# Kernel optimization log

Hardware: AMD Instinct MI355X
Metric: run time of the kernel (lower is better)

## Reference

```python
import jax, jax.numpy as jnp
import numpy as np

B, T, OBS = 256, 200, 128
H, L, S = 128, 32, 50


def setup_inputs() -> dict:
    key = jax.random.key(0)
    ks = jax.random.split(key, 10)
    sc_in = 1.0 / np.sqrt(OBS + L)
    sc_h = 1.0 / np.sqrt(H)
    return {
        "inputs": jax.random.normal(ks[0], (B, T, OBS), dtype=jnp.float32),
        "eps": jax.random.normal(ks[1], (T, B * S, L), dtype=jnp.float32),
        "W_ih": jax.random.normal(ks[2], (4 * H, OBS + L), dtype=jnp.float32) * sc_in,
        "W_hh": jax.random.normal(ks[3], (4 * H, H), dtype=jnp.float32) * sc_h,
        "b_ih": jax.random.normal(ks[4], (4 * H,), dtype=jnp.float32) * 0.01,
        "b_hh": jax.random.normal(ks[5], (4 * H,), dtype=jnp.float32) * 0.01,
        "W_mu": jax.random.normal(ks[6], (L, H), dtype=jnp.float32) * sc_h,
        "b_mu": jax.random.normal(ks[7], (L,), dtype=jnp.float32) * 0.01,
        "cov_diag": jax.random.uniform(ks[8], (L,), dtype=jnp.float32, minval=0.5, maxval=1.5),
        "num_samples": S,
    }


def reference(inputs, eps, W_ih, W_hh, b_ih, b_hh, W_mu, b_mu, cov_diag, num_samples):
    batch, num_steps, _ = inputs.shape
    hid = b_ih.shape[0] // 4
    lat = b_mu.shape[0]
    BS = batch * num_samples

    std = jnp.sqrt(cov_diag)                       # [L], state-independent diag cov
    logdet = jnp.sum(jnp.log(cov_diag))
    TWO_PI = 2.0 * jnp.pi
    ent_const = 0.5 * lat * (1.0 + jnp.log(TWO_PI)) + 0.5 * logdet

    # tile([num_samples, 1]) in torch repeats the whole batch block -> sample-major
    x_tiled = jnp.tile(inputs.transpose(1, 0, 2), (1, num_samples, 1))  # [T, BS, obs]

    def step(carry, xs):
        h, c, z_prev = carry
        x_t, eps_t = xs
        rnn_in = jnp.concatenate([x_t, z_prev], axis=-1)          # [BS, obs+L]
        gates = rnn_in @ W_ih.T + b_ih + h @ W_hh.T + b_hh        # [BS, 4H]
        i, f, g, o = jnp.split(gates, 4, axis=-1)
        c_new = jax.nn.sigmoid(f) * c + jax.nn.sigmoid(i) * jnp.tanh(g)
        h_new = jax.nn.sigmoid(o) * jnp.tanh(c_new)
        mean = h_new @ W_mu.T + b_mu                              # [BS, L]
        z = mean + eps_t * std                                    # reparam sample
        ent = jnp.broadcast_to(ent_const, (z.shape[0],))          # diag-MVN entropy
        # log N(z; mean, diag(cov)) with (z-mean)/std == eps_t
        lp = -0.5 * (jnp.sum(eps_t * eps_t, axis=-1) + lat * jnp.log(TWO_PI) + logdet)
        return (h_new, c_new, z), (z, ent, lp)

    init = (
        jnp.zeros((BS, hid), dtype=inputs.dtype),
        jnp.zeros((BS, hid), dtype=inputs.dtype),
        jnp.zeros((BS, lat), dtype=inputs.dtype),
    )
    _, (zs, ents, lps) = jax.lax.scan(step, init, (x_tiled, eps))  # [T,BS,L],[T,BS],[T,BS]

    sampled_s = zs.transpose(1, 0, 2).reshape(num_samples, batch, num_steps, lat)
    entropies = ents.T.reshape(num_samples, batch, num_steps)
    log_probs = lps.T.reshape(num_samples, batch, num_steps)
    return sampled_s, entropies, log_probs
```

## Files before the change

### kernel.cpp

```cpp
#include <hip/hip_runtime.h>
#include <stdint.h>

#define T_STEPS 200
#define OBSD    128
#define HID     128
#define LATD    32
#define BS_TOT  12800
#define KIN     160

#define OUT_ENT_OFF 81920000
#define OUT_LP_OFF  84480000

#define WR_OFF  0
#define H_OFF   131072
#define WMU_OFF 147456
#define E_OFF   155648
#define LDS_SZ  159744

#define L2E  1.4426950408889634f
#define L2E2 2.8853900817779268f
#define LOG2PI 1.8378770664093453f

typedef short  bf16x8 __attribute__((ext_vector_type(8)));
typedef float  f32x4  __attribute__((ext_vector_type(4)));
typedef uint32_t u32;

__device__ __forceinline__ uint16_t f2bf(float f) {
    u32 u = __builtin_bit_cast(u32, f);
    u32 r = (u + 0x7fffu + ((u >> 16) & 1u)) >> 16;
    return (uint16_t)r;
}
__device__ __forceinline__ float bf2f(u32 bits16) {
    u32 u = bits16 << 16;
    return __builtin_bit_cast(float, u);
}
__device__ __forceinline__ u32 pack2(float a, float b) {
    return (u32)f2bf(a) | ((u32)f2bf(b) << 16);
}
__device__ __forceinline__ u32 cvt_pk_bf16(float lo, float hi) {
    u32 r;
    asm("v_cvt_pk_bf16_f32 %0, %1, %2" : "=v"(r) : "v"(lo), "v"(hi));
    return r;
}
__device__ __forceinline__ float sig2(float x) {
    float e;
    asm("v_exp_f32 %0, -%1" : "=v"(e) : "v"(x));
    return __builtin_amdgcn_rcpf(1.f + e);
}
__device__ __forceinline__ float tanh2(float x) {
    float e;
    asm("v_exp_f32 %0, %1" : "=v"(e) : "v"(x));
    return 1.f - 2.f * __builtin_amdgcn_rcpf(1.f + e);
}
__device__ __forceinline__ int hswz(int row, int col) {
    return ((row << 8) + (col << 1)) ^ ((row & 7) << 4);
}

__global__ __launch_bounds__(512, 2) void xg_prep(
    const float* __restrict__ x,
    const float* __restrict__ W_ih,
    const float* __restrict__ b_ih,
    const float* __restrict__ b_hh,
    const float* __restrict__ b_mu,
    uint16_t* __restrict__ xg)
{
    const int blk = blockIdx.x;
    const int t   = blk >> 2, bq = blk & 3;
    const int tid = threadIdx.x;
    const int w = tid >> 6, l = tid & 63, lg = l >> 4, ln = l & 15;
    const int b0 = bq * 64;

    bf16x8 wb[4][4];
    float  bias[4];
    #pragma unroll
    for (int q = 0; q < 4; ++q) {
        const int col = q * 128 + w * 16 + ln;
        float zb = 0.f;
        #pragma unroll
        for (int j = 0; j < 32; ++j) zb += b_mu[j] * W_ih[col * KIN + 128 + j];
        bias[q] = b_ih[col] + b_hh[col] + (t > 0 ? zb : 0.f);
        #pragma unroll
        for (int ks = 0; ks < 4; ++ks) {
            bf16x8 v;
            #pragma unroll
            for (int e = 0; e < 8; ++e)
                v[e] = (short)f2bf(W_ih[col * KIN + ks * 32 + lg * 8 + e]);
            wb[ks][q] = v;
        }
    }

    f32x4 acc[4][4];
    const f32x4 vz = {0.f, 0.f, 0.f, 0.f};
    #pragma unroll
    for (int rt = 0; rt < 4; ++rt)
        #pragma unroll
        for (int q = 0; q < 4; ++q) acc[rt][q] = vz;

    #pragma unroll
    for (int ks = 0; ks < 4; ++ks) {
        bf16x8 a[4];
        #pragma unroll
        for (int rt = 0; rt < 4; ++rt) {
            const int brow = b0 + rt * 16 + ln;
            const float* src = x + ((size_t)brow * T_STEPS + t) * OBSD + ks * 32 + lg * 8;
            bf16x8 v;
            #pragma unroll
            for (int e = 0; e < 8; ++e) v[e] = (short)f2bf(src[e]);
            a[rt] = v;
        }
        #pragma unroll
        for (int rt = 0; rt < 4; ++rt)
            #pragma unroll
            for (int q = 0; q < 4; ++q)
                acc[rt][q] = __builtin_amdgcn_mfma_f32_16x16x32_bf16(
                    a[rt], wb[ks][q], acc[rt][q], 0, 0, 0);
    }

    const float gsc[4] = {L2E, L2E, L2E2, L2E};
    uint4* dst = (uint4*)xg + ((size_t)blk * 512 + tid) * 8;
    #pragma unroll
    for (int rt = 0; rt < 4; ++rt) {
        float v0[4], v1[4], v2[4], v3[4];
        #pragma unroll
        for (int e = 0; e < 4; ++e) {
            v0[e] = (acc[rt][0][e] + bias[0]) * gsc[0];
            v1[e] = (acc[rt][1][e] + bias[1]) * gsc[1];
            v2[e] = (acc[rt][2][e] + bias[2]) * gsc[2];
            v3[e] = (acc[rt][3][e] + bias[3]) * gsc[3];
        }
        uint4 o0, o1;
        o0.x = pack2(v0[0], v0[1]); o0.y = pack2(v0[2], v0[3]);
        o0.z = pack2(v1[0], v1[1]); o0.w = pack2(v1[2], v1[3]);
        o1.x = pack2(v2[0], v2[1]); o1.y = pack2(v2[2], v2[3]);
        o1.z = pack2(v3[0], v3[1]); o1.w = pack2(v3[2], v3[3]);
        dst[2 * rt]     = o0;
        dst[2 * rt + 1] = o1;
    }
}

__global__ __launch_bounds__(256) void lp_ent(
    const float* __restrict__ eps,
    const float* __restrict__ cov,
    float* __restrict__ out)
{
    const int blk = blockIdx.x;
    const int rc = blk >> 2, tq = blk & 3;
    const int tid = threadIdx.x;
    const int c = tid & 3, rl = tid >> 2;
    const int row = rc * 64 + rl;

    float logdet = 0.f;
    for (int i = 0; i < LATD; ++i) logdet += logf(cov[i]);
    const float lconst = 32.f * LOG2PI + logdet;
    const float ec = 0.5f * 32.f * (1.f + LOG2PI) + 0.5f * logdet;

    const int t0 = tq * 50;
    for (int t = t0; t < t0 + 50; ++t) {
        const float* ep = eps + ((size_t)t * BS_TOT + row) * LATD + c * 8;
        const float4 a0 = *(const float4*)ep;
        const float4 a1 = *(const float4*)(ep + 4);
        float ps = a0.x*a0.x + a0.y*a0.y + a0.z*a0.z + a0.w*a0.w
                 + a1.x*a1.x + a1.y*a1.y + a1.z*a1.z + a1.w*a1.w;
        ps += __shfl_xor(ps, 1, 64);
        ps += __shfl_xor(ps, 2, 64);
        if (c == 0) {
            out[OUT_LP_OFF  + (size_t)row * 200 + t] = -0.5f * (ps + lconst);
            out[OUT_ENT_OFF + (size_t)row * 200 + t] = ec;
        }
    }
}

__global__ __launch_bounds__(1024, 4) void lstm_main(
    const float* __restrict__ eps,
    const float* __restrict__ W_ih,
    const float* __restrict__ W_hh,
    const float* __restrict__ W_mu,
    const float* __restrict__ b_mu,
    const float* __restrict__ cov,
    const uint16_t* __restrict__ xg,
    float* __restrict__ out)
{
    __shared__ __align__(16) char smem[LDS_SZ];

    const int tid = threadIdx.x;
    const int w = tid >> 6, l = tid & 63, lg = l >> 4, ln = l & 15;
    const int wp = w & 7, half = w >> 3;

    const int xcd = blockIdx.x & 7;
    const int wk  = (xcd >> 1) + 4 * ((blockIdx.x >> 3) + 25 * (xcd & 1));
    const int bq  = wk & 3;
    const int bs0 = wk * 64;

    {
        float* ws = (float*)(smem + H_OFF);
        for (int i = tid; i < 4096; i += 1024) ws[i] = W_mu[i];
    }
    __syncthreads();
    const float* wmu_s = (const float*)(smem + H_OFF);

    for (int i = tid; i < 2048; i += 1024) {
        const int col = i >> 6, k2 = (i & 63) * 2;
        const u32 p = pack2(wmu_s[col * HID + k2], wmu_s[col * HID + k2 + 1]);
        *(u32*)(smem + WMU_OFF + (((col << 8) + (k2 << 1)) ^ ((col & 7) << 4))) = p;
    }

    bf16x8 weg[4];
    {
        float stds[8];
        #pragma unroll
        for (int e = 0; e < 8; ++e) stds[e] = sqrtf(cov[lg * 8 + e]);
        const float gsc[4] = {L2E, L2E, L2E2, L2E};
        #pragma unroll
        for (int q = 0; q < 4; ++q) {
            const int col = q * 128 + wp * 16 + ln;
            bf16x8 v;
            #pragma unroll
            for (int e = 0; e < 8; ++e)
                v[e] = (short)f2bf(W_ih[col * KIN + 128 + lg * 8 + e] * stds[e] * gsc[q]);
            weg[q] = v;
        }
    }

    #pragma unroll
    for (int qq = 0; qq < 2; ++qq) {
        const int q = half * 2 + qq;
        const float gs = (q == 2) ? L2E2 : L2E;
        const int col = q * 128 + wp * 16 + ln;
        float wzf[32];
        #pragma unroll
        for (int j4 = 0; j4 < 8; ++j4)
            *(float4*)&wzf[j4 * 4] = *(const float4*)&W_ih[col * KIN + 128 + j4 * 4];
        #pragma unroll
        for (int ks = 0; ks < 4; ++ks) {
            float base[8];
            *(float4*)&base[0] = *(const float4*)&W_hh[col * HID + ks * 32 + lg * 8];
            *(float4*)&base[4] = *(const float4*)&W_hh[col * HID + ks * 32 + lg * 8 + 4];
            bf16x8 v;
            #pragma unroll
            for (int e = 0; e < 8; ++e) {
                float s = base[e];
                #pragma unroll
                for (int j = 0; j < 32; ++j)
                    s += wzf[j] * wmu_s[j * HID + ks * 32 + lg * 8 + e];
                v[e] = (short)f2bf(s * gs);
            }
            *(bf16x8*)(smem + WR_OFF + (((ks * 4 + q) * 8 + wp) << 10) + l * 16) = v;
        }
    }

    const int rtm = (w >> 1) & 3, ctm = w & 1;
    const int zcol = ctm * 16 + ln;
    const float stdv = sqrtf(cov[zcol]);
    const float bmu  = b_mu[zcol];

    __syncthreads();

    for (int i = tid; i < 4096; i += 1024) ((u32*)(smem + H_OFF))[i] = 0;
    for (int i = tid; i < 1024; i += 1024) ((u32*)(smem + E_OFF))[i] = 0;

    const f32x4 vz4 = {0.f, 0.f, 0.f, 0.f};
    f32x4 cst[2] = {vz4, vz4};

    const int erow = tid >> 4, ecol = (tid & 15) * 2;
    const int ewr = ((erow >> 4) * 64 + (ecol >> 3) * 16 + (erow & 15)) * 16 + (ecol & 7) * 2;

    __syncthreads();

    for (int t = 0; t < T_STEPS; ++t) {
        uint4 xv[4];
        const uint4* xp = (const uint4*)xg
            + ((size_t)(t * 4 + bq) * 512 + wp * 64 + l) * 8 + half * 4;
        #pragma unroll
        for (int i = 0; i < 4; ++i) xv[i] = xp[i];
        const float2 fev = *(const float2*)(eps + ((size_t)t * BS_TOT + bs0 + erow) * LATD + ecol);

        f32x4 acc[2][4];
        #pragma unroll
        for (int rt = 0; rt < 2; ++rt) {
            const bf16x8 aE = *(const bf16x8*)(smem + E_OFF + (((half * 2 + rt) * 64 + l) << 4));
            #pragma unroll
            for (int q = 0; q < 4; ++q)
                acc[rt][q] = __builtin_amdgcn_mfma_f32_16x16x32_bf16(
                    aE, weg[q], vz4, 0, 0, 0);
        }
        #pragma unroll
        for (int ks = 0; ks < 4; ++ks) {
            bf16x8 bfr[4];
            #pragma unroll
            for (int q = 0; q < 4; ++q)
                bfr[q] = *(const bf16x8*)(smem + WR_OFF + (((ks * 4 + q) * 8 + wp) << 10) + l * 16);
            bf16x8 a[2];
            #pragma unroll
            for (int rt = 0; rt < 2; ++rt)
                a[rt] = *(const bf16x8*)(smem + H_OFF + hswz((half * 2 + rt) * 16 + ln, ks * 32 + lg * 8));
            #pragma unroll
            for (int rt = 0; rt < 2; ++rt)
                #pragma unroll
                for (int q = 0; q < 4; ++q)
                    acc[rt][q] = __builtin_amdgcn_mfma_f32_16x16x32_bf16(
                        a[rt], bfr[q], acc[rt][q], 0, 0, 0);
        }
        if (half == 0 && t > 0) {
            f32x4 macc = vz4;
            #pragma unroll
            for (int ks = 0; ks < 4; ++ks) {
                const bf16x8 am = *(const bf16x8*)(smem + H_OFF + hswz(rtm * 16 + ln, ks * 32 + lg * 8));
                const bf16x8 bm = *(const bf16x8*)(smem + WMU_OFF + hswz(zcol, ks * 32 + lg * 8));
                macc = __builtin_amdgcn_mfma_f32_16x16x32_bf16(am, bm, macc, 0, 0, 0);
            }
            #pragma unroll
            for (int e = 0; e < 4; ++e) {
                const int row = rtm * 16 + lg * 4 + e;
                const int eb = (rtm * 64 + (zcol >> 3) * 16 + (lg * 4 + e)) * 16 + (zcol & 7) * 2;
                const float evv = bf2f(*(const uint16_t*)(smem + E_OFF + eb));
                out[(size_t)(bs0 + row) * 6400 + (t - 1) * 32 + zcol] =
                    macc[e] + bmu + evv * stdv;
            }
        }

        __syncthreads();

        *(u32*)(smem + E_OFF + ewr) = cvt_pk_bf16(fev.x, fev.y);

        #pragma unroll
        for (int rt = 0; rt < 2; ++rt) {
            const uint4 u01 = xv[2 * rt], u23 = xv[2 * rt + 1];
            const float xi[4] = { bf2f(u01.x & 0xffff), bf2f(u01.x >> 16),
                                  bf2f(u01.y & 0xffff), bf2f(u01.y >> 16) };
            const float xf[4] = { bf2f(u01.z & 0xffff), bf2f(u01.z >> 16),
                                  bf2f(u01.w & 0xffff), bf2f(u01.w >> 16) };
            const float xgv[4] = { bf2f(u23.x & 0xffff), bf2f(u23.x >> 16),
                                   bf2f(u23.y & 0xffff), bf2f(u23.y >> 16) };
            const float xo[4] = { bf2f(u23.z & 0xffff), bf2f(u23.z >> 16),
                                  bf2f(u23.w & 0xffff), bf2f(u23.w >> 16) };
            #pragma unroll
            for (int e = 0; e < 4; ++e) {
                const float iv = acc[rt][0][e] + xi[e];
                const float fv = acc[rt][1][e] + xf[e];
                const float gv = acc[rt][2][e] + xgv[e];
                const float ov = acc[rt][3][e] + xo[e];
                const float c  = sig2(fv) * cst[rt][e] + sig2(iv) * tanh2(gv);
                cst[rt][e] = c;
                const float h = sig2(ov) * tanh2(c * L2E2);
                const int row = (half * 2 + rt) * 16 + lg * 4 + e;
                *(uint16_t*)(smem + H_OFF + hswz(row, wp * 16 + ln)) = f2bf(h);
            }
        }

        __syncthreads();
    }

    if (half == 0) {
        f32x4 macc = vz4;
        #pragma unroll
        for (int ks = 0; ks < 4; ++ks) {
            const bf16x8 am = *(const bf16x8*)(smem + H_OFF + hswz(rtm * 16 + ln, ks * 32 + lg * 8));
            const bf16x8 bm = *(const bf16x8*)(smem + WMU_OFF + hswz(zcol, ks * 32 + lg * 8));
            macc = __builtin_amdgcn_mfma_f32_16x16x32_bf16(am, bm, macc, 0, 0, 0);
        }
        #pragma unroll
        for (int e = 0; e < 4; ++e) {
            const int row = rtm * 16 + lg * 4 + e;
            const int eb = (rtm * 64 + (zcol >> 3) * 16 + (lg * 4 + e)) * 16 + (zcol & 7) * 2;
            const float evv = bf2f(*(const uint16_t*)(smem + E_OFF + eb));
            out[(size_t)(bs0 + row) * 6400 + 199 * 32 + zcol] =
                macc[e] + bmu + evv * stdv;
        }
    }
}

extern "C" void kernel_launch(void* const* d_in, const int* in_sizes, int n_in,
                              void* d_out, int out_size, void* d_ws, size_t ws_size,
                              hipStream_t stream) {
    const float* x    = (const float*)d_in[0];
    const float* eps  = (const float*)d_in[1];
    const float* W_ih = (const float*)d_in[2];
    const float* W_hh = (const float*)d_in[3];
    const float* b_ih = (const float*)d_in[4];
    const float* b_hh = (const float*)d_in[5];
    const float* W_mu = (const float*)d_in[6];
    const float* b_mu = (const float*)d_in[7];
    const float* cov  = (const float*)d_in[8];
    float* out = (float*)d_out;
    uint16_t* xg = (uint16_t*)d_ws;

    hipLaunchKernelGGL(xg_prep, dim3(800), dim3(512), 0, stream, x, W_ih, b_ih, b_hh, b_mu, xg);
    hipLaunchKernelGGL(lp_ent, dim3(800), dim3(256), 0, stream, eps, cov, out);
    hipLaunchKernelGGL(lstm_main, dim3(200), dim3(1024), 0, stream,
                       eps, W_ih, W_hh, W_mu, b_mu, cov, xg, out);
}
```

Measured before the change: 1.811 ms.

## Hold recurrent weights in registers with 512-thread blocks and double-buffered LDS

The LSTM recurrence kernel drops from 16 to 8 waves per block. Each wave now covers all 64 rows and keeps its fused W_hh+W_ih·W_mu slice in registers (wr[4][4]) instead of reading it from LDS every step. The hidden-state and eps tiles are double-buffered in LDS, so the two per-step __syncthreads become a single lgkmcnt wait plus barrier. This removes weight LDS traffic and one barrier per timestep. In exchange it raises register pressure, since accumulators, cell state and x loads all double, and halves thread-level parallelism.

```diff
diff --git a/kernel.cpp b/kernel.cpp
--- a/kernel.cpp
+++ b/kernel.cpp
@@ -11,11 +11,10 @@
 #define OUT_ENT_OFF 81920000
 #define OUT_LP_OFF  84480000
 
-#define WR_OFF  0
-#define H_OFF   131072
-#define WMU_OFF 147456
-#define E_OFF   155648
-#define LDS_SZ  159744
+#define H0_OFF  0
+#define WMU_OFF 32768
+#define E0_OFF  40960
+#define LDS_SZ  49152
 
 #define L2E  1.4426950408889634f
 #define L2E2 2.8853900817779268f
@@ -24,6 +23,13 @@
 typedef short  bf16x8 __attribute__((ext_vector_type(8)));
 typedef float  f32x4  __attribute__((ext_vector_type(4)));
 typedef uint32_t u32;
+
+#define BAR() do {                                        \
+    __builtin_amdgcn_sched_barrier(0);                    \
+    asm volatile("s_waitcnt lgkmcnt(0)" ::: "memory");    \
+    __builtin_amdgcn_s_barrier();                         \
+    __builtin_amdgcn_sched_barrier(0);                    \
+} while (0)
 
 __device__ __forceinline__ uint16_t f2bf(float f) {
     u32 u = __builtin_bit_cast(u32, f);
@@ -170,7 +176,7 @@
     }
 }
 
-__global__ __launch_bounds__(1024, 4) void lstm_main(
+__global__ __launch_bounds__(512, 2) void lstm_main(
     const float* __restrict__ eps,
     const float* __restrict__ W_ih,
     const float* __restrict__ W_hh,
@@ -184,7 +190,6 @@
 
     const int tid = threadIdx.x;
     const int w = tid >> 6, l = tid & 63, lg = l >> 4, ln = l & 15;
-    const int wp = w & 7, half = w >> 3;
 
     const int xcd = blockIdx.x & 7;
     const int wk  = (xcd >> 1) + 4 * ((blockIdx.x >> 3) + 25 * (xcd & 1));
@@ -192,13 +197,13 @@
     const int bs0 = wk * 64;
 
     {
-        float* ws = (float*)(smem + H_OFF);
-        for (int i = tid; i < 4096; i += 1024) ws[i] = W_mu[i];
+        float* ws = (float*)(smem + H0_OFF);
+        for (int i = tid; i < 4096; i += 512) ws[i] = W_mu[i];
     }
     __syncthreads();
-    const float* wmu_s = (const float*)(smem + H_OFF);
-
-    for (int i = tid; i < 2048; i += 1024) {
+    const float* wmu_s = (const float*)(smem + H0_OFF);
+
+    for (int i = tid; i < 2048; i += 512) {
         const int col = i >> 6, k2 = (i & 63) * 2;
         const u32 p = pack2(wmu_s[col * HID + k2], wmu_s[col * HID + k2 + 1]);
         *(u32*)(smem + WMU_OFF + (((col << 8) + (k2 << 1)) ^ ((col & 7) << 4))) = p;
@@ -212,7 +217,7 @@
         const float gsc[4] = {L2E, L2E, L2E2, L2E};
         #pragma unroll
         for (int q = 0; q < 4; ++q) {
-            const int col = q * 128 + wp * 16 + ln;
+            const int col = q * 128 + w * 16 + ln;
             bf16x8 v;
             #pragma unroll
             for (int e = 0; e < 8; ++e)
@@ -221,11 +226,11 @@
         }
     }
 
+    bf16x8 wr[4][4];
     #pragma unroll
-    for (int qq = 0; qq < 2; ++qq) {
-        const int q = half * 2 + qq;
+    for (int q = 0; q < 4; ++q) {
         const float gs = (q == 2) ? L2E2 : L2E;
-        const int col = q * 128 + wp * 16 + ln;
+        const int col = q * 128 + w * 16 + ln;
         float wzf[32];
         #pragma unroll
         for (int j4 = 0; j4 < 8; ++j4)
@@ -244,40 +249,46 @@
                     s += wzf[j] * wmu_s[j * HID + ks * 32 + lg * 8 + e];
                 v[e] = (short)f2bf(s * gs);
             }
-            *(bf16x8*)(smem + WR_OFF + (((ks * 4 + q) * 8 + wp) << 10) + l * 16) = v;
-        }
-    }
-
-    const int rtm = (w >> 1) & 3, ctm = w & 1;
+            wr[ks][q] = v;
+        }
+    }
+
+    const int rtm = w >> 1, ctm = w & 1;
     const int zcol = ctm * 16 + ln;
     const float stdv = sqrtf(cov[zcol]);
     const float bmu  = b_mu[zcol];
 
     __syncthreads();
 
-    for (int i = tid; i < 4096; i += 1024) ((u32*)(smem + H_OFF))[i] = 0;
-    for (int i = tid; i < 1024; i += 1024) ((u32*)(smem + E_OFF))[i] = 0;
+    for (int i = tid; i < 4096; i += 512) ((u32*)(smem + H0_OFF))[i] = 0;
+    for (int i = tid; i < 1024; i += 512) ((u32*)(smem + E0_OFF))[i] = 0;
 
     const f32x4 vz4 = {0.f, 0.f, 0.f, 0.f};
-    f32x4 cst[2] = {vz4, vz4};
-
-    const int erow = tid >> 4, ecol = (tid & 15) * 2;
-    const int ewr = ((erow >> 4) * 64 + (ecol >> 3) * 16 + (erow & 15)) * 16 + (ecol & 7) * 2;
+    f32x4 cst[4] = {vz4, vz4, vz4, vz4};
+
+    const int erow = tid >> 3, ecol = (tid & 7) * 4;
+    const int ert = erow >> 4;
+    const int ewr = ((ert * 64 + (ecol >> 3) * 16 + (erow & 15)) << 4) + (ecol & 7) * 2;
 
     __syncthreads();
 
     for (int t = 0; t < T_STEPS; ++t) {
-        uint4 xv[4];
-        const uint4* xp = (const uint4*)xg
-            + ((size_t)(t * 4 + bq) * 512 + wp * 64 + l) * 8 + half * 4;
-        #pragma unroll
-        for (int i = 0; i < 4; ++i) xv[i] = xp[i];
-        const float2 fev = *(const float2*)(eps + ((size_t)t * BS_TOT + bs0 + erow) * LATD + ecol);
-
-        f32x4 acc[2][4];
-        #pragma unroll
-        for (int rt = 0; rt < 2; ++rt) {
-            const bf16x8 aE = *(const bf16x8*)(smem + E_OFF + (((half * 2 + rt) * 64 + l) << 4));
+        const int pb = t & 1;
+        const char* Hp = smem + H0_OFF + pb * 16384;
+        char*       Hn = smem + H0_OFF + (pb ^ 1) * 16384;
+        const char* Ep = smem + E0_OFF + pb * 4096;
+        char*       En = smem + E0_OFF + (pb ^ 1) * 4096;
+
+        uint4 xv[8];
+        const uint4* xp = (const uint4*)xg + ((size_t)(t * 4 + bq) * 512 + tid) * 8;
+        #pragma unroll
+        for (int i = 0; i < 8; ++i) xv[i] = xp[i];
+        const float4 fe = *(const float4*)(eps + ((size_t)t * BS_TOT + bs0 + erow) * LATD + ecol);
+
+        f32x4 acc[4][4];
+        #pragma unroll
+        for (int rt = 0; rt < 4; ++rt) {
+            const bf16x8 aE = *(const bf16x8*)(Ep + ((rt * 64 + l) << 4));
             #pragma unroll
             for (int q = 0; q < 4; ++q)
                 acc[rt][q] = __builtin_amdgcn_mfma_f32_16x16x32_bf16(
@@ -285,45 +296,37 @@
         }
         #pragma unroll
         for (int ks = 0; ks < 4; ++ks) {
-            bf16x8 bfr[4];
-            #pragma unroll
-            for (int q = 0; q < 4; ++q)
-                bfr[q] = *(const bf16x8*)(smem + WR_OFF + (((ks * 4 + q) * 8 + wp) << 10) + l * 16);
-            bf16x8 a[2];
-            #pragma unroll
-            for (int rt = 0; rt < 2; ++rt)
-                a[rt] = *(const bf16x8*)(smem + H_OFF + hswz((half * 2 + rt) * 16 + ln, ks * 32 + lg * 8));
-            #pragma unroll
-            for (int rt = 0; rt < 2; ++rt)
+            bf16x8 a[4];
+            #pragma unroll
+            for (int rt = 0; rt < 4; ++rt)
+                a[rt] = *(const bf16x8*)(Hp + hswz(rt * 16 + ln, ks * 32 + lg * 8));
+            #pragma unroll
+            for (int rt = 0; rt < 4; ++rt)
                 #pragma unroll
                 for (int q = 0; q < 4; ++q)
                     acc[rt][q] = __builtin_amdgcn_mfma_f32_16x16x32_bf16(
-                        a[rt], bfr[q], acc[rt][q], 0, 0, 0);
-        }
-        if (half == 0 && t > 0) {
+                        a[rt], wr[ks][q], acc[rt][q], 0, 0, 0);
+        }
+        if (t > 0) {
             f32x4 macc = vz4;
             #pragma unroll
             for (int ks = 0; ks < 4; ++ks) {
-                const bf16x8 am = *(const bf16x8*)(smem + H_OFF + hswz(rtm * 16 + ln, ks * 32 + lg * 8));
+                const bf16x8 am = *(const bf16x8*)(Hp + hswz(rtm * 16 + ln, ks * 32 + lg * 8));
                 const bf16x8 bm = *(const bf16x8*)(smem + WMU_OFF + hswz(zcol, ks * 32 + lg * 8));
                 macc = __builtin_amdgcn_mfma_f32_16x16x32_bf16(am, bm, macc, 0, 0, 0);
             }
             #pragma unroll
             for (int e = 0; e < 4; ++e) {
                 const int row = rtm * 16 + lg * 4 + e;
-                const int eb = (rtm * 64 + (zcol >> 3) * 16 + (lg * 4 + e)) * 16 + (zcol & 7) * 2;
-                const float evv = bf2f(*(const uint16_t*)(smem + E_OFF + eb));
+                const float evv = bf2f(*(const uint16_t*)(
+                    Ep + ((rtm * 64 + (zcol >> 3) * 16 + (lg * 4 + e)) << 4) + (zcol & 7) * 2));
                 out[(size_t)(bs0 + row) * 6400 + (t - 1) * 32 + zcol] =
                     macc[e] + bmu + evv * stdv;
             }
         }
 
-        __syncthreads();
-
-        *(u32*)(smem + E_OFF + ewr) = cvt_pk_bf16(fev.x, fev.y);
-
-        #pragma unroll
-        for (int rt = 0; rt < 2; ++rt) {
+        #pragma unroll
+        for (int rt = 0; rt < 4; ++rt) {
             const uint4 u01 = xv[2 * rt], u23 = xv[2 * rt + 1];
             const float xi[4] = { bf2f(u01.x & 0xffff), bf2f(u01.x >> 16),
                                   bf2f(u01.y & 0xffff), bf2f(u01.y >> 16) };
@@ -342,27 +345,36 @@
                 const float c  = sig2(fv) * cst[rt][e] + sig2(iv) * tanh2(gv);
                 cst[rt][e] = c;
                 const float h = sig2(ov) * tanh2(c * L2E2);
-                const int row = (half * 2 + rt) * 16 + lg * 4 + e;
-                *(uint16_t*)(smem + H_OFF + hswz(row, wp * 16 + ln)) = f2bf(h);
+                const int row = rt * 16 + lg * 4 + e;
+                *(uint16_t*)(Hn + hswz(row, w * 16 + ln)) = f2bf(h);
             }
         }
 
-        __syncthreads();
-    }
-
-    if (half == 0) {
+        {
+            uint2 p;
+            p.x = cvt_pk_bf16(fe.x, fe.y);
+            p.y = cvt_pk_bf16(fe.z, fe.w);
+            *(uint2*)(En + ewr) = p;
+        }
+
+        BAR();
+    }
+
+    {
+        const char* Hp = smem + H0_OFF + (T_STEPS & 1) * 16384;
+        const char* Ep = smem + E0_OFF + (T_STEPS & 1) * 4096;
         f32x4 macc = vz4;
         #pragma unroll
         for (int ks = 0; ks < 4; ++ks) {
-            const bf16x8 am = *(const bf16x8*)(smem + H_OFF + hswz(rtm * 16 + ln, ks * 32 + lg * 8));
+            const bf16x8 am = *(const bf16x8*)(Hp + hswz(rtm * 16 + ln, ks * 32 + lg * 8));
             const bf16x8 bm = *(const bf16x8*)(smem + WMU_OFF + hswz(zcol, ks * 32 + lg * 8));
             macc = __builtin_amdgcn_mfma_f32_16x16x32_bf16(am, bm, macc, 0, 0, 0);
         }
         #pragma unroll
         for (int e = 0; e < 4; ++e) {
             const int row = rtm * 16 + lg * 4 + e;
-            const int eb = (rtm * 64 + (zcol >> 3) * 16 + (lg * 4 + e)) * 16 + (zcol & 7) * 2;
-            const float evv = bf2f(*(const uint16_t*)(smem + E_OFF + eb));
+            const float evv = bf2f(*(const uint16_t*)(
+                Ep + ((rtm * 64 + (zcol >> 3) * 16 + (lg * 4 + e)) << 4) + (zcol & 7) * 2));
             out[(size_t)(bs0 + row) * 6400 + 199 * 32 + zcol] =
                 macc[e] + bmu + evv * stdv;
         }
@@ -386,6 +398,6 @@
 
     hipLaunchKernelGGL(xg_prep, dim3(800), dim3(512), 0, stream, x, W_ih, b_ih, b_hh, b_mu, xg);
     hipLaunchKernelGGL(lp_ent, dim3(800), dim3(256), 0, stream, eps, cov, out);
-    hipLaunchKernelGGL(lstm_main, dim3(200), dim3(1024), 0, stream,
+    hipLaunchKernelGGL(lstm_main, dim3(200), dim3(512), 0, stream,
                        eps, W_ih, W_hh, W_mu, b_mu, cov, xg, out);
 }
```

New measurement: 1.824 ms. No clear change (+0.7%).

## Fuse lp/entropy into LSTM grid, double-buffer h, hold weights in registers

Applied to the files above, without the earlier changes.

Removes the separate lp_ent kernel and runs its work on 56 extra blocks of the main LSTM launch, using CUs left idle by the 200 recurrent blocks. The recurrent loop double-buffers the h state in LDS so each step needs one barrier instead of two. Eps is now fed to the MFMA from registers instead of staged through LDS, and the xg precomputed gates are folded in as the MFMA accumulator init. Half of the recurrent weight tiles move from LDS into registers to cut LDS traffic. This raises register pressure and removes the dependency ordering between the two former kernels.

```diff
diff --git a/kernel.cpp b/kernel.cpp
--- a/kernel.cpp
+++ b/kernel.cpp
@@ -12,10 +12,9 @@
 #define OUT_LP_OFF  84480000
 
 #define WR_OFF  0
-#define H_OFF   131072
-#define WMU_OFF 147456
-#define E_OFF   155648
-#define LDS_SZ  159744
+#define H_OFF   65536
+#define WMU_OFF 98304
+#define LDS_SZ  106496
 
 #define L2E  1.4426950408889634f
 #define L2E2 2.8853900817779268f
@@ -24,6 +23,14 @@
 typedef short  bf16x8 __attribute__((ext_vector_type(8)));
 typedef float  f32x4  __attribute__((ext_vector_type(4)));
 typedef uint32_t u32;
+typedef u32    u32x4  __attribute__((ext_vector_type(4)));
+
+#define BAR() do {                                        \
+    __builtin_amdgcn_sched_barrier(0);                    \
+    asm volatile("s_waitcnt lgkmcnt(0)" ::: "memory");    \
+    __builtin_amdgcn_s_barrier();                         \
+    __builtin_amdgcn_sched_barrier(0);                    \
+} while (0)
 
 __device__ __forceinline__ uint16_t f2bf(float f) {
     u32 u = __builtin_bit_cast(u32, f);
@@ -54,6 +61,14 @@
 }
 __device__ __forceinline__ int hswz(int row, int col) {
     return ((row << 8) + (col << 1)) ^ ((row & 7) << 4);
+}
+__device__ __forceinline__ f32x4 cfrag(u32 u01, u32 u23) {
+    f32x4 c;
+    c[0] = __builtin_bit_cast(float, u01 << 16);
+    c[1] = __builtin_bit_cast(float, u01 & 0xffff0000u);
+    c[2] = __builtin_bit_cast(float, u23 << 16);
+    c[3] = __builtin_bit_cast(float, u23 & 0xffff0000u);
+    return c;
 }
 
 __global__ __launch_bounds__(512, 2) void xg_prep(
@@ -138,38 +153,6 @@
     }
 }
 
-__global__ __launch_bounds__(256) void lp_ent(
-    const float* __restrict__ eps,
-    const float* __restrict__ cov,
-    float* __restrict__ out)
-{
-    const int blk = blockIdx.x;
-    const int rc = blk >> 2, tq = blk & 3;
-    const int tid = threadIdx.x;
-    const int c = tid & 3, rl = tid >> 2;
-    const int row = rc * 64 + rl;
-
-    float logdet = 0.f;
-    for (int i = 0; i < LATD; ++i) logdet += logf(cov[i]);
-    const float lconst = 32.f * LOG2PI + logdet;
-    const float ec = 0.5f * 32.f * (1.f + LOG2PI) + 0.5f * logdet;
-
-    const int t0 = tq * 50;
-    for (int t = t0; t < t0 + 50; ++t) {
-        const float* ep = eps + ((size_t)t * BS_TOT + row) * LATD + c * 8;
-        const float4 a0 = *(const float4*)ep;
-        const float4 a1 = *(const float4*)(ep + 4);
-        float ps = a0.x*a0.x + a0.y*a0.y + a0.z*a0.z + a0.w*a0.w
-                 + a1.x*a1.x + a1.y*a1.y + a1.z*a1.z + a1.w*a1.w;
-        ps += __shfl_xor(ps, 1, 64);
-        ps += __shfl_xor(ps, 2, 64);
-        if (c == 0) {
-            out[OUT_LP_OFF  + (size_t)row * 200 + t] = -0.5f * (ps + lconst);
-            out[OUT_ENT_OFF + (size_t)row * 200 + t] = ec;
-        }
-    }
-}
-
 __global__ __launch_bounds__(1024, 4) void lstm_main(
     const float* __restrict__ eps,
     const float* __restrict__ W_ih,
@@ -183,6 +166,28 @@
     __shared__ __align__(16) char smem[LDS_SZ];
 
     const int tid = threadIdx.x;
+
+    if (blockIdx.x >= 200) {
+        float logdet = 0.f;
+        for (int i = 0; i < LATD; ++i) logdet += logf(cov[i]);
+        const float lconst = 32.f * LOG2PI + logdet;
+        const float ec = 0.5f * 32.f * (1.f + LOG2PI) + 0.5f * logdet;
+        const int base = (blockIdx.x - 200) * 1024 + tid;
+        for (int j = base; j < T_STEPS * BS_TOT; j += 56 * 1024) {
+            const float* ep = eps + (size_t)j * LATD;
+            float ps = 0.f;
+            #pragma unroll
+            for (int k = 0; k < 8; ++k) {
+                const float4 a = *(const float4*)(ep + k * 4);
+                ps += a.x * a.x + a.y * a.y + a.z * a.z + a.w * a.w;
+            }
+            const int t = j / BS_TOT, row = j - t * BS_TOT;
+            out[OUT_LP_OFF  + (size_t)row * 200 + t] = -0.5f * (ps + lconst);
+            out[OUT_ENT_OFF + (size_t)row * 200 + t] = ec;
+        }
+        return;
+    }
+
     const int w = tid >> 6, l = tid & 63, lg = l >> 4, ln = l & 15;
     const int wp = w & 7, half = w >> 3;
 
@@ -221,9 +226,9 @@
         }
     }
 
+    bf16x8 wrr[2][4];
     #pragma unroll
-    for (int qq = 0; qq < 2; ++qq) {
-        const int q = half * 2 + qq;
+    for (int q = 0; q < 4; ++q) {
         const float gs = (q == 2) ? L2E2 : L2E;
         const int col = q * 128 + wp * 16 + ln;
         float wzf[32];
@@ -232,6 +237,7 @@
             *(float4*)&wzf[j4 * 4] = *(const float4*)&W_ih[col * KIN + 128 + j4 * 4];
         #pragma unroll
         for (int ks = 0; ks < 4; ++ks) {
+            if (ks < 2 && half != 0) continue;
             float base[8];
             *(float4*)&base[0] = *(const float4*)&W_hh[col * HID + ks * 32 + lg * 8];
             *(float4*)&base[4] = *(const float4*)&W_hh[col * HID + ks * 32 + lg * 8 + 4];
@@ -244,7 +250,10 @@
                     s += wzf[j] * wmu_s[j * HID + ks * 32 + lg * 8 + e];
                 v[e] = (short)f2bf(s * gs);
             }
-            *(bf16x8*)(smem + WR_OFF + (((ks * 4 + q) * 8 + wp) << 10) + l * 16) = v;
+            if (ks < 2)
+                *(bf16x8*)(smem + WR_OFF + (((ks * 4 + q) * 8 + wp) << 10) + l * 16) = v;
+            else
+                wrr[ks - 2][q] = v;
         }
     }
 
@@ -256,114 +265,128 @@
     __syncthreads();
 
     for (int i = tid; i < 4096; i += 1024) ((u32*)(smem + H_OFF))[i] = 0;
-    for (int i = tid; i < 1024; i += 1024) ((u32*)(smem + E_OFF))[i] = 0;
 
     const f32x4 vz4 = {0.f, 0.f, 0.f, 0.f};
     f32x4 cst[2] = {vz4, vz4};
-
-    const int erow = tid >> 4, ecol = (tid & 15) * 2;
-    const int ewr = ((erow >> 4) * 64 + (ecol >> 3) * 16 + (erow & 15)) * 16 + (ecol & 7) * 2;
+    u32x4 epf[2] = {{0, 0, 0, 0}, {0, 0, 0, 0}};
 
     __syncthreads();
 
     for (int t = 0; t < T_STEPS; ++t) {
+        const int pb = t & 1;
+        const char* Hp = smem + H_OFF + pb * 16384;
+        char*       Hn = smem + H_OFF + (pb ^ 1) * 16384;
+
         uint4 xv[4];
         const uint4* xp = (const uint4*)xg
             + ((size_t)(t * 4 + bq) * 512 + wp * 64 + l) * 8 + half * 4;
         #pragma unroll
         for (int i = 0; i < 4; ++i) xv[i] = xp[i];
-        const float2 fev = *(const float2*)(eps + ((size_t)t * BS_TOT + bs0 + erow) * LATD + ecol);
+        float4 fa[2], fb[2];
+        #pragma unroll
+        for (int rt = 0; rt < 2; ++rt) {
+            const float* ep = eps
+                + ((size_t)t * BS_TOT + bs0 + (half * 2 + rt) * 16 + ln) * LATD + lg * 8;
+            fa[rt] = *(const float4*)ep;
+            fb[rt] = *(const float4*)(ep + 4);
+        }
+        float ez[4];
+        if (half == 0) {
+            const size_t eb = (size_t)(t > 0 ? t - 1 : 0) * BS_TOT + bs0 + rtm * 16 + lg * 4;
+            #pragma unroll
+            for (int e = 0; e < 4; ++e) ez[e] = eps[(eb + e) * LATD + zcol];
+        }
 
         f32x4 acc[2][4];
         #pragma unroll
         for (int rt = 0; rt < 2; ++rt) {
-            const bf16x8 aE = *(const bf16x8*)(smem + E_OFF + (((half * 2 + rt) * 64 + l) << 4));
-            #pragma unroll
-            for (int q = 0; q < 4; ++q)
-                acc[rt][q] = __builtin_amdgcn_mfma_f32_16x16x32_bf16(
-                    aE, weg[q], vz4, 0, 0, 0);
+            const bf16x8 aE = __builtin_bit_cast(bf16x8, epf[rt]);
+            const uint4 ua = xv[2 * rt], ub = xv[2 * rt + 1];
+            acc[rt][0] = __builtin_amdgcn_mfma_f32_16x16x32_bf16(aE, weg[0], cfrag(ua.x, ua.y), 0, 0, 0);
+            acc[rt][1] = __builtin_amdgcn_mfma_f32_16x16x32_bf16(aE, weg[1], cfrag(ua.z, ua.w), 0, 0, 0);
+            acc[rt][2] = __builtin_amdgcn_mfma_f32_16x16x32_bf16(aE, weg[2], cfrag(ub.x, ub.y), 0, 0, 0);
+            acc[rt][3] = __builtin_amdgcn_mfma_f32_16x16x32_bf16(aE, weg[3], cfrag(ub.z, ub.w), 0, 0, 0);
         }
         #pragma unroll
         for (int ks = 0; ks < 4; ++ks) {
-            bf16x8 bfr[4];
-            #pragma unroll
-            for (int q = 0; q < 4; ++q)
-                bfr[q] = *(const bf16x8*)(smem + WR_OFF + (((ks * 4 + q) * 8 + wp) << 10) + l * 16);
             bf16x8 a[2];
             #pragma unroll
             for (int rt = 0; rt < 2; ++rt)
-                a[rt] = *(const bf16x8*)(smem + H_OFF + hswz((half * 2 + rt) * 16 + ln, ks * 32 + lg * 8));
-            #pragma unroll
-            for (int rt = 0; rt < 2; ++rt)
+                a[rt] = *(const bf16x8*)(Hp + hswz((half * 2 + rt) * 16 + ln, ks * 32 + lg * 8));
+            #pragma unroll
+            for (int q = 0; q < 4; ++q) {
+                bf16x8 bfr;
+                if (ks < 2)
+                    bfr = *(const bf16x8*)(smem + WR_OFF + (((ks * 4 + q) * 8 + wp) << 10) + l * 16);
+                else
+                    bfr = wrr[ks - 2][q];
                 #pragma unroll
-                for (int q = 0; q < 4; ++q)
+                for (int rt = 0; rt < 2; ++rt)
                     acc[rt][q] = __builtin_amdgcn_mfma_f32_16x16x32_bf16(
-                        a[rt], bfr[q], acc[rt][q], 0, 0, 0);
+                        a[rt], bfr, acc[rt][q], 0, 0, 0);
+            }
         }
         if (half == 0 && t > 0) {
             f32x4 macc = vz4;
             #pragma unroll
             for (int ks = 0; ks < 4; ++ks) {
-                const bf16x8 am = *(const bf16x8*)(smem + H_OFF + hswz(rtm * 16 + ln, ks * 32 + lg * 8));
+                const bf16x8 am = *(const bf16x8*)(Hp + hswz(rtm * 16 + ln, ks * 32 + lg * 8));
                 const bf16x8 bm = *(const bf16x8*)(smem + WMU_OFF + hswz(zcol, ks * 32 + lg * 8));
                 macc = __builtin_amdgcn_mfma_f32_16x16x32_bf16(am, bm, macc, 0, 0, 0);
             }
             #pragma unroll
+            for (int e = 0; e < 4; ++e)
+                out[(size_t)(bs0 + rtm * 16 + lg * 4 + e) * 6400 + (t - 1) * 32 + zcol] =
+                    macc[e] + bmu + ez[e] * stdv;
+        }
+
+        #pragma unroll
+        for (int rt = 0; rt < 2; ++rt) {
+            float hv[4];
+            #pragma unroll
             for (int e = 0; e < 4; ++e) {
-                const int row = rtm * 16 + lg * 4 + e;
-                const int eb = (rtm * 64 + (zcol >> 3) * 16 + (lg * 4 + e)) * 16 + (zcol & 7) * 2;
-                const float evv = bf2f(*(const uint16_t*)(smem + E_OFF + eb));
-                out[(size_t)(bs0 + row) * 6400 + (t - 1) * 32 + zcol] =
-                    macc[e] + bmu + evv * stdv;
+                const float c = sig2(acc[rt][1][e]) * cst[rt][e]
+                              + sig2(acc[rt][0][e]) * tanh2(acc[rt][2][e]);
+                cst[rt][e] = c;
+                hv[e] = sig2(acc[rt][3][e]) * tanh2(c * L2E2);
             }
-        }
-
-        __syncthreads();
-
-        *(u32*)(smem + E_OFF + ewr) = cvt_pk_bf16(fev.x, fev.y);
+            const u32 p01 = cvt_pk_bf16(hv[0], hv[1]);
+            const u32 p23 = cvt_pk_bf16(hv[2], hv[3]);
+            const int r0 = (half * 2 + rt) * 16 + lg * 4;
+            const int hc = wp * 16 + ln;
+            *(uint16_t*)(Hn + hswz(r0,     hc)) = (uint16_t)p01;
+            *(uint16_t*)(Hn + hswz(r0 + 1, hc)) = (uint16_t)(p01 >> 16);
+            *(uint16_t*)(Hn + hswz(r0 + 2, hc)) = (uint16_t)p23;
+            *(uint16_t*)(Hn + hswz(r0 + 3, hc)) = (uint16_t)(p23 >> 16);
+        }
 
         #pragma unroll
         for (int rt = 0; rt < 2; ++rt) {
-            const uint4 u01 = xv[2 * rt], u23 = xv[2 * rt + 1];
-            const float xi[4] = { bf2f(u01.x & 0xffff), bf2f(u01.x >> 16),
-                                  bf2f(u01.y & 0xffff), bf2f(u01.y >> 16) };
-            const float xf[4] = { bf2f(u01.z & 0xffff), bf2f(u01.z >> 16),
-                                  bf2f(u01.w & 0xffff), bf2f(u01.w >> 16) };
-            const float xgv[4] = { bf2f(u23.x & 0xffff), bf2f(u23.x >> 16),
-                                   bf2f(u23.y & 0xffff), bf2f(u23.y >> 16) };
-            const float xo[4] = { bf2f(u23.z & 0xffff), bf2f(u23.z >> 16),
-                                  bf2f(u23.w & 0xffff), bf2f(u23.w >> 16) };
-            #pragma unroll
-            for (int e = 0; e < 4; ++e) {
-                const float iv = acc[rt][0][e] + xi[e];
-                const float fv = acc[rt][1][e] + xf[e];
-                const float gv = acc[rt][2][e] + xgv[e];
-                const float ov = acc[rt][3][e] + xo[e];
-                const float c  = sig2(fv) * cst[rt][e] + sig2(iv) * tanh2(gv);
-                cst[rt][e] = c;
-                const float h = sig2(ov) * tanh2(c * L2E2);
-                const int row = (half * 2 + rt) * 16 + lg * 4 + e;
-                *(uint16_t*)(smem + H_OFF + hswz(row, wp * 16 + ln)) = f2bf(h);
-            }
-        }
-
-        __syncthreads();
+            u32x4 pk;
+            pk[0] = cvt_pk_bf16(fa[rt].x, fa[rt].y);
+            pk[1] = cvt_pk_bf16(fa[rt].z, fa[rt].w);
+            pk[2] = cvt_pk_bf16(fb[rt].x, fb[rt].y);
+            pk[3] = cvt_pk_bf16(fb[rt].z, fb[rt].w);
+            epf[rt] = pk;
+        }
+
+        BAR();
     }
 
     if (half == 0) {
+        const char* Hp = smem + H_OFF;
         f32x4 macc = vz4;
         #pragma unroll
         for (int ks = 0; ks < 4; ++ks) {
-            const bf16x8 am = *(const bf16x8*)(smem + H_OFF + hswz(rtm * 16 + ln, ks * 32 + lg * 8));
+            const bf16x8 am = *(const bf16x8*)(Hp + hswz(rtm * 16 + ln, ks * 32 + lg * 8));
             const bf16x8 bm = *(const bf16x8*)(smem + WMU_OFF + hswz(zcol, ks * 32 + lg * 8));
             macc = __builtin_amdgcn_mfma_f32_16x16x32_bf16(am, bm, macc, 0, 0, 0);
         }
+        const size_t eb = (size_t)199 * BS_TOT + bs0 + rtm * 16 + lg * 4;
         #pragma unroll
         for (int e = 0; e < 4; ++e) {
-            const int row = rtm * 16 + lg * 4 + e;
-            const int eb = (rtm * 64 + (zcol >> 3) * 16 + (lg * 4 + e)) * 16 + (zcol & 7) * 2;
-            const float evv = bf2f(*(const uint16_t*)(smem + E_OFF + eb));
-            out[(size_t)(bs0 + row) * 6400 + 199 * 32 + zcol] =
+            const float evv = eps[(eb + e) * LATD + zcol];
+            out[(size_t)(bs0 + rtm * 16 + lg * 4 + e) * 6400 + 199 * 32 + zcol] =
                 macc[e] + bmu + evv * stdv;
         }
     }
@@ -385,7 +408,6 @@
     uint16_t* xg = (uint16_t*)d_ws;
 
     hipLaunchKernelGGL(xg_prep, dim3(800), dim3(512), 0, stream, x, W_ih, b_ih, b_hh, b_mu, xg);
-    hipLaunchKernelGGL(lp_ent, dim3(800), dim3(256), 0, stream, eps, cov, out);
-    hipLaunchKernelGGL(lstm_main, dim3(200), dim3(1024), 0, stream,
+    hipLaunchKernelGGL(lstm_main, dim3(256), dim3(1024), 0, stream,
                        eps, W_ih, W_hh, W_mu, b_mu, cov, xg, out);
 }
```

New measurement: 4.175 ms. 131% more time.
